# Kernel optimization log

Measured on AMD Instinct MI355X. Metric: run time of the kernel, lower is better.

The kernel has to match this reference:

```python
import jax, jax.numpy as jnp
import numpy as np

B, CH1, CH2, HID, T, E = 64, 3, 4, 16, 16384, 512

def setup_inputs() -> dict:
    key = jax.random.key(0)
    ks = jax.random.split(key, 12)
    s_t = 1.0 / np.sqrt(T)   # fan_in = input_dim for q/k/v projections
    s_e = 1.0 / np.sqrt(E)   # fan_in = embed_dim for out_proj
    return {
        "x":  jax.random.normal(ks[0], (B, 7, T), jnp.float32),
        "W1": jax.random.normal(ks[1], (HID, CH1), jnp.float32) / np.sqrt(CH1),
        "W2": jax.random.normal(ks[2], (HID, CH2), jnp.float32) / np.sqrt(CH2),
        "Wq": jax.random.normal(ks[3], (E, T), jnp.float32) * s_t,
        "bq": jnp.zeros((E,), jnp.float32),
        "Wk": jax.random.normal(ks[4], (E, T), jnp.float32) * s_t,
        "bk": jnp.zeros((E,), jnp.float32),
        "Wv": jax.random.normal(ks[5], (E, T), jnp.float32) * s_t,
        "bv": jnp.zeros((E,), jnp.float32),
        "Wo": jax.random.normal(ks[6], (T, E), jnp.float32) * s_e,
        "bo": jnp.zeros((T,), jnp.float32),
        "W3": jax.random.normal(ks[7], (CH1, HID), jnp.float32) / np.sqrt(HID),
    }

def reference(x, W1, W2, Wq, bq, Wk, bk, Wv, bv, Wo, bo, W3):
    p = x[:, :CH1]            # [B,3,T]  narrow(1,0,ch_1)
    c = x[:, 3:3 + CH2]       # [B,4,T]  narrow(1,3,ch_2)
    q = jnp.einsum('oc,bct->bot', W1, p)   # fc_1: [B,16,T]
    cc = jnp.einsum('oc,bct->bot', W2, c)  # fc_2: [B,16,T]
    # CrossAttention: Linears act on last dim (T -> E)
    Q = jnp.einsum('bct,et->bce', q, Wq) + bq    # [B,16,E]
    K = jnp.einsum('bct,et->bce', cc, Wk) + bk   # [B,16,E]
    V = jnp.einsum('bct,et->bce', cc, Wv) + bv   # [B,16,E]
    scale = 1.0 / np.sqrt(HID)                   # nch = 16 query channels
    attn_w = jax.nn.softmax(jnp.einsum('bce,bcf->bef', Q, K) * scale, axis=-1)  # [B,E,E]
    attn = jnp.einsum('bef,bcf->bce', attn_w, V)  # [B,16,E]
    out = jnp.einsum('bce,te->bct', attn, Wo) + bo  # out_proj: [B,16,T]
    y = jnp.einsum('oc,bct->bot', W3, out)          # fc_3: [B,3,T]
    return p + y
```

## Files before the change

### kernel.cpp

```cpp
#include <hip/hip_runtime.h>

#define BB 64
#define TT 16384
#define EE 512

typedef _Float16 half8 __attribute__((ext_vector_type(8)));
typedef float floatx4 __attribute__((ext_vector_type(4)));

static __device__ __forceinline__ half8 cvt_half8(float4 a, float4 b) {
  half8 h;
  h[0] = (_Float16)a.x; h[1] = (_Float16)a.y; h[2] = (_Float16)a.z; h[3] = (_Float16)a.w;
  h[4] = (_Float16)b.x; h[5] = (_Float16)b.y; h[6] = (_Float16)b.z; h[7] = (_Float16)b.w;
  return h;
}

__global__ __launch_bounds__(256) void zero_ws(float4* __restrict__ p) {
  p[blockIdx.x * 256 + threadIdx.x] = (float4){0.f, 0.f, 0.f, 0.f};
}

__global__ __launch_bounds__(256) void proj_gemm(
    const float* __restrict__ x, const float* __restrict__ Wa,
    const float* __restrict__ Wb, float* __restrict__ outC,
    int chan_base, int chan_per_b, int ldout)
{
  __shared__ _Float16 As[64][40];
  __shared__ _Float16 Bs[128][40];
  const int t = threadIdx.x;
  const int wave = t >> 6, lane = t & 63;
  const int quad = lane >> 4, l16 = lane & 15;
  const int mtile = blockIdx.y, ntile = blockIdx.x;
  const int k0 = blockIdx.z << 10;

  const int arow = t >> 2, akk = (t & 3) << 3;
  const int r = mtile * 64 + arow;
  const int bidx = r / chan_per_b;
  const int j = r - bidx * chan_per_b;
  const float* aptr = x + (size_t)(bidx * 7 + chan_base + j) * TT + k0 + akk;

  const int brow = t >> 1, bkk = (t & 1) << 4;
  const int ncol = ntile * 128 + brow;
  const float* wsrc = (ncol < EE) ? Wa : Wb;
  const float* bptr = wsrc + (size_t)(ncol & (EE - 1)) * TT + k0 + bkk;

  floatx4 acc[4][2];
  for (int rt = 0; rt < 4; ++rt)
    for (int ct = 0; ct < 2; ++ct)
      acc[rt][ct] = (floatx4){0.f, 0.f, 0.f, 0.f};

  for (int kt = 0; kt < 32; ++kt) {
    __syncthreads();
    float4 a0 = *(const float4*)aptr;
    float4 a1 = *(const float4*)(aptr + 4);
    float4 b0 = *(const float4*)bptr;
    float4 b1 = *(const float4*)(bptr + 4);
    float4 b2 = *(const float4*)(bptr + 8);
    float4 b3 = *(const float4*)(bptr + 12);
    *(half8*)&As[arow][akk]     = cvt_half8(a0, a1);
    *(half8*)&Bs[brow][bkk]     = cvt_half8(b0, b1);
    *(half8*)&Bs[brow][bkk + 8] = cvt_half8(b2, b3);
    aptr += 32; bptr += 32;
    __syncthreads();
    half8 bf0 = *(const half8*)&Bs[wave * 32 + l16][quad * 8];
    half8 bf1 = *(const half8*)&Bs[wave * 32 + 16 + l16][quad * 8];
#pragma unroll
    for (int rt = 0; rt < 4; ++rt) {
      half8 af = *(const half8*)&As[rt * 16 + l16][quad * 8];
      acc[rt][0] = __builtin_amdgcn_mfma_f32_16x16x32_f16(af, bf0, acc[rt][0], 0, 0, 0);
      acc[rt][1] = __builtin_amdgcn_mfma_f32_16x16x32_f16(af, bf1, acc[rt][1], 0, 0, 0);
    }
  }
#pragma unroll
  for (int rt = 0; rt < 4; ++rt) {
#pragma unroll
    for (int ct = 0; ct < 2; ++ct) {
      const int gr = mtile * 64 + rt * 16 + quad * 4;
      const int gc = ntile * 128 + wave * 32 + ct * 16 + l16;
#pragma unroll
      for (int rg = 0; rg < 4; ++rg)
        atomicAdd(&outC[(size_t)(gr + rg) * ldout + gc], acc[rt][ct][rg]);
    }
  }
}

__global__ __launch_bounds__(256) void attn_mid(
    const float* __restrict__ Xq, const float* __restrict__ Xkv,
    const float* __restrict__ W1, const float* __restrict__ W2,
    const float* __restrict__ W3,
    const float* __restrict__ bq, const float* __restrict__ bk,
    const float* __restrict__ bv, _Float16* __restrict__ U)
{
  __shared__ float Ks[16][512];
  __shared__ float VW[3][512];
  __shared__ float Qs[16][64];
  __shared__ float Xs[4][512];
  __shared__ float W1s[48], W2s[64], W3s[48], W32s[12], w3sum[3];
  const int t = threadIdx.x;
  const int b = blockIdx.y;
  const int e0 = blockIdx.x * 64;

  if (t < 48) W1s[t] = W1[t];
  if (t >= 64 && t < 128) W2s[t - 64] = W2[t - 64];
  if (t >= 128 && t < 176) W3s[t - 128] = W3[t - 128];
  __syncthreads();
  if (t < 12) {
    const int o = t >> 2, jj = t & 3;
    float s = 0.f;
    for (int c = 0; c < 16; ++c) s += W3s[o * 16 + c] * W2s[c * 4 + jj];
    W32s[t] = s;
  }
  if (t >= 16 && t < 19) {
    const int o = t - 16;
    float s = 0.f;
    for (int c = 0; c < 16; ++c) s += W3s[o * 16 + c];
    w3sum[o] = s;
  }
  for (int i = t; i < 2048; i += 256) {
    const int jj = i >> 9, f = i & 511;
    Xs[jj][f] = Xkv[(size_t)(b * 4 + jj) * 1024 + f];
  }
  __syncthreads();
  for (int i = t; i < 8192; i += 256) {
    const int c = i >> 9, f = i & 511;
    float s = bk[f];
#pragma unroll
    for (int jj = 0; jj < 4; ++jj) s += W2s[c * 4 + jj] * Xs[jj][f];
    Ks[c][f] = s;
  }
  __syncthreads();
  for (int i = t; i < 2048; i += 256) {
    const int jj = i >> 9, f = i & 511;
    Xs[jj][f] = Xkv[(size_t)(b * 4 + jj) * 1024 + 512 + f];
  }
  __syncthreads();
  for (int i = t; i < 1536; i += 256) {
    const int o = i >> 9, f = i & 511;
    float s = w3sum[o] * bv[f];
#pragma unroll
    for (int jj = 0; jj < 4; ++jj) s += W32s[o * 4 + jj] * Xs[jj][f];
    VW[o][f] = s;
  }
  for (int i = t; i < 1024; i += 256) {
    const int c = i >> 6, el = i & 63;
    float s = bq[e0 + el];
#pragma unroll
    for (int jj = 0; jj < 3; ++jj)
      s += W1s[c * 3 + jj] * Xq[(size_t)(b * 3 + jj) * 512 + e0 + el];
    Qs[c][el] = s;
  }
  __syncthreads();

  const int wave = t >> 6, lane = t & 63;
  float vwr[3][8];
#pragma unroll
  for (int o = 0; o < 3; ++o) {
    float4 va = *(const float4*)&VW[o][lane * 8];
    float4 vb = *(const float4*)&VW[o][lane * 8 + 4];
    vwr[o][0] = va.x; vwr[o][1] = va.y; vwr[o][2] = va.z; vwr[o][3] = va.w;
    vwr[o][4] = vb.x; vwr[o][5] = vb.y; vwr[o][6] = vb.z; vwr[o][7] = vb.w;
  }

  for (int g = 0; g < 4; ++g) {
    const int el0 = wave * 16 + g * 4;
    float s[4][8];
#pragma unroll
    for (int e = 0; e < 4; ++e)
#pragma unroll
      for (int i = 0; i < 8; ++i) s[e][i] = 0.f;
#pragma unroll
    for (int c = 0; c < 16; ++c) {
      float4 k0 = *(const float4*)&Ks[c][lane * 8];
      float4 k1 = *(const float4*)&Ks[c][lane * 8 + 4];
      float4 qv = *(const float4*)&Qs[c][el0];
      float qa[4] = {qv.x, qv.y, qv.z, qv.w};
#pragma unroll
      for (int e = 0; e < 4; ++e) {
        const float q = qa[e];
        s[e][0] += q * k0.x; s[e][1] += q * k0.y; s[e][2] += q * k0.z; s[e][3] += q * k0.w;
        s[e][4] += q * k1.x; s[e][5] += q * k1.y; s[e][6] += q * k1.z; s[e][7] += q * k1.w;
      }
    }
#pragma unroll
    for (int e = 0; e < 4; ++e) {
      float mx = s[e][0];
#pragma unroll
      for (int i = 1; i < 8; ++i) mx = fmaxf(mx, s[e][i]);
#pragma unroll
      for (int off = 32; off; off >>= 1) mx = fmaxf(mx, __shfl_xor(mx, off));
      float p[8], sum = 0.f;
#pragma unroll
      for (int i = 0; i < 8; ++i) { p[i] = __expf(0.25f * (s[e][i] - mx)); sum += p[i]; }
      float u0 = 0.f, u1 = 0.f, u2 = 0.f;
#pragma unroll
      for (int i = 0; i < 8; ++i) {
        u0 += p[i] * vwr[0][i];
        u1 += p[i] * vwr[1][i];
        u2 += p[i] * vwr[2][i];
      }
#pragma unroll
      for (int off = 32; off; off >>= 1) {
        sum += __shfl_xor(sum, off);
        u0  += __shfl_xor(u0, off);
        u1  += __shfl_xor(u1, off);
        u2  += __shfl_xor(u2, off);
      }
      if (lane == 0) {
        const float inv = 1.0f / sum;
        const size_t base = (size_t)b * 3 * 512 + (e0 + el0 + e);
        U[base]        = (_Float16)(u0 * inv);
        U[base + 512]  = (_Float16)(u1 * inv);
        U[base + 1024] = (_Float16)(u2 * inv);
      }
    }
  }
}

__global__ __launch_bounds__(256) void out_gemm(
    const _Float16* __restrict__ U, const float* __restrict__ Wo,
    const float* __restrict__ x, const float* __restrict__ bo,
    const float* __restrict__ W3, float* __restrict__ outY)
{
  __shared__ _Float16 As[64][40];
  __shared__ _Float16 Bs[128][40];
  __shared__ float w3sh[3];
  const int t = threadIdx.x;
  const int wave = t >> 6, lane = t & 63;
  const int quad = lane >> 4, l16 = lane & 15;
  const int mtile = blockIdx.y, ntile = blockIdx.x;
  if (t < 3) {
    float s = 0.f;
    for (int c = 0; c < 16; ++c) s += W3[t * 16 + c];
    w3sh[t] = s;
  }
  const int arow = t >> 2, akk = (t & 3) << 3;
  const _Float16* aptr = U + (size_t)(mtile * 64 + arow) * EE + akk;
  const int brow = t >> 1, bkk = (t & 1) << 4;
  const float* bptr = Wo + (size_t)(ntile * 128 + brow) * EE + bkk;

  floatx4 acc[4][2];
  for (int rt = 0; rt < 4; ++rt)
    for (int ct = 0; ct < 2; ++ct)
      acc[rt][ct] = (floatx4){0.f, 0.f, 0.f, 0.f};

  for (int kt = 0; kt < 16; ++kt) {
    __syncthreads();
    half8 av = *(const half8*)aptr;
    float4 b0 = *(const float4*)bptr;
    float4 b1 = *(const float4*)(bptr + 4);
    float4 b2 = *(const float4*)(bptr + 8);
    float4 b3 = *(const float4*)(bptr + 12);
    *(half8*)&As[arow][akk]     = av;
    *(half8*)&Bs[brow][bkk]     = cvt_half8(b0, b1);
    *(half8*)&Bs[brow][bkk + 8] = cvt_half8(b2, b3);
    aptr += 32; bptr += 32;
    __syncthreads();
    half8 bf0 = *(const half8*)&Bs[wave * 32 + l16][quad * 8];
    half8 bf1 = *(const half8*)&Bs[wave * 32 + 16 + l16][quad * 8];
#pragma unroll
    for (int rt = 0; rt < 4; ++rt) {
      half8 af = *(const half8*)&As[rt * 16 + l16][quad * 8];
      acc[rt][0] = __builtin_amdgcn_mfma_f32_16x16x32_f16(af, bf0, acc[rt][0], 0, 0, 0);
      acc[rt][1] = __builtin_amdgcn_mfma_f32_16x16x32_f16(af, bf1, acc[rt][1], 0, 0, 0);
    }
  }
#pragma unroll
  for (int rt = 0; rt < 4; ++rt) {
#pragma unroll
    for (int ct = 0; ct < 2; ++ct) {
      const int gr = mtile * 64 + rt * 16 + quad * 4;
      const int tc = ntile * 128 + wave * 32 + ct * 16 + l16;
      const float bot = bo[tc];
#pragma unroll
      for (int rg = 0; rg < 4; ++rg) {
        const int rr = gr + rg;
        const int bb = rr / 3, oo = rr - bb * 3;
        const float v = acc[rt][ct][rg]
                      + x[(size_t)(bb * 7 + oo) * TT + tc]
                      + w3sh[oo] * bot;
        outY[(size_t)rr * TT + tc] = v;
      }
    }
  }
}

extern "C" void kernel_launch(void* const* d_in, const int* in_sizes, int n_in,
                              void* d_out, int out_size, void* d_ws, size_t ws_size,
                              hipStream_t stream) {
  const float* x  = (const float*)d_in[0];
  const float* W1 = (const float*)d_in[1];
  const float* W2 = (const float*)d_in[2];
  const float* Wq = (const float*)d_in[3];
  const float* bq = (const float*)d_in[4];
  const float* Wk = (const float*)d_in[5];
  const float* bk = (const float*)d_in[6];
  const float* Wv = (const float*)d_in[7];
  const float* bv = (const float*)d_in[8];
  const float* Wo = (const float*)d_in[9];
  const float* bo = (const float*)d_in[10];
  const float* W3 = (const float*)d_in[11];
  float* out = (float*)d_out;

  char* ws = (char*)d_ws;
  float* Xq      = (float*)ws;
  float* Xkv     = (float*)(ws + 393216);
  _Float16* U    = (_Float16*)(ws + 1441792);

  zero_ws<<<dim3(352), 256, 0, stream>>>((float4*)ws);

  proj_gemm<<<dim3(4, 3, 16), 256, 0, stream>>>(x, Wq, Wq, Xq, 0, 3, 512);
  proj_gemm<<<dim3(8, 4, 16), 256, 0, stream>>>(x, Wk, Wv, Xkv, 3, 4, 1024);
  attn_mid<<<dim3(8, BB), 256, 0, stream>>>(Xq, Xkv, W1, W2, W3, bq, bk, bv, U);
  out_gemm<<<dim3(128, 3), 256, 0, stream>>>(U, Wo, x, bo, W3, out);
}
```

Baseline: 314.1 us.

## Merge projection launches, deepen split-K, prefetch tiles, halve out_gemm N-tile

```diff
diff --git a/kernel.cpp b/kernel.cpp
--- a/kernel.cpp
+++ b/kernel.cpp
@@ -19,22 +19,36 @@
 }
 
 __global__ __launch_bounds__(256) void proj_gemm(
-    const float* __restrict__ x, const float* __restrict__ Wa,
-    const float* __restrict__ Wb, float* __restrict__ outC,
-    int chan_base, int chan_per_b, int ldout)
+    const float* __restrict__ x, const float* __restrict__ Wq,
+    const float* __restrict__ Wk, const float* __restrict__ Wv,
+    float* __restrict__ Xq, float* __restrict__ Xkv)
 {
   __shared__ _Float16 As[64][40];
   __shared__ _Float16 Bs[128][40];
   const int t = threadIdx.x;
   const int wave = t >> 6, lane = t & 63;
   const int quad = lane >> 4, l16 = lane & 15;
-  const int mtile = blockIdx.y, ntile = blockIdx.x;
-  const int k0 = blockIdx.z << 10;
+
+  const int tile = blockIdx.x;
+  int mtile, ntile, chan_base, cpb, ldout;
+  const float *Wa, *Wb;
+  float* outC;
+  if (tile < 12) {
+    mtile = tile >> 2; ntile = tile & 3;
+    chan_base = 0; cpb = 3; ldout = 512;
+    Wa = Wq; Wb = Wq; outC = Xq;
+  } else {
+    const int t2 = tile - 12;
+    mtile = t2 >> 3; ntile = t2 & 7;
+    chan_base = 3; cpb = 4; ldout = 1024;
+    Wa = Wk; Wb = Wv; outC = Xkv;
+  }
+  const int k0 = blockIdx.y << 9;
 
   const int arow = t >> 2, akk = (t & 3) << 3;
   const int r = mtile * 64 + arow;
-  const int bidx = r / chan_per_b;
-  const int j = r - bidx * chan_per_b;
+  const int bidx = r / cpb;
+  const int j = r - bidx * cpb;
   const float* aptr = x + (size_t)(bidx * 7 + chan_base + j) * TT + k0 + akk;
 
   const int brow = t >> 1, bkk = (t & 1) << 4;
@@ -47,19 +61,31 @@
     for (int ct = 0; ct < 2; ++ct)
       acc[rt][ct] = (floatx4){0.f, 0.f, 0.f, 0.f};
 
-  for (int kt = 0; kt < 32; ++kt) {
+  float4 a0 = *(const float4*)aptr;
+  float4 a1 = *(const float4*)(aptr + 4);
+  float4 b0 = *(const float4*)bptr;
+  float4 b1 = *(const float4*)(bptr + 4);
+  float4 b2 = *(const float4*)(bptr + 8);
+  float4 b3 = *(const float4*)(bptr + 12);
+
+  for (int kt = 0; kt < 16; ++kt) {
+    const half8 ha  = cvt_half8(a0, a1);
+    const half8 hb0 = cvt_half8(b0, b1);
+    const half8 hb1 = cvt_half8(b2, b3);
     __syncthreads();
-    float4 a0 = *(const float4*)aptr;
-    float4 a1 = *(const float4*)(aptr + 4);
-    float4 b0 = *(const float4*)bptr;
-    float4 b1 = *(const float4*)(bptr + 4);
-    float4 b2 = *(const float4*)(bptr + 8);
-    float4 b3 = *(const float4*)(bptr + 12);
-    *(half8*)&As[arow][akk]     = cvt_half8(a0, a1);
-    *(half8*)&Bs[brow][bkk]     = cvt_half8(b0, b1);
-    *(half8*)&Bs[brow][bkk + 8] = cvt_half8(b2, b3);
-    aptr += 32; bptr += 32;
+    *(half8*)&As[arow][akk]     = ha;
+    *(half8*)&Bs[brow][bkk]     = hb0;
+    *(half8*)&Bs[brow][bkk + 8] = hb1;
     __syncthreads();
+    if (kt < 15) {
+      aptr += 32; bptr += 32;
+      a0 = *(const float4*)aptr;
+      a1 = *(const float4*)(aptr + 4);
+      b0 = *(const float4*)bptr;
+      b1 = *(const float4*)(bptr + 4);
+      b2 = *(const float4*)(bptr + 8);
+      b3 = *(const float4*)(bptr + 12);
+    }
     half8 bf0 = *(const half8*)&Bs[wave * 32 + l16][quad * 8];
     half8 bf1 = *(const half8*)&Bs[wave * 32 + 16 + l16][quad * 8];
 #pragma unroll
@@ -220,7 +246,7 @@
     const float* __restrict__ W3, float* __restrict__ outY)
 {
   __shared__ _Float16 As[64][40];
-  __shared__ _Float16 Bs[128][40];
+  __shared__ _Float16 Bs[64][40];
   __shared__ float w3sh[3];
   const int t = threadIdx.x;
   const int wave = t >> 6, lane = t & 63;
@@ -233,51 +259,49 @@
   }
   const int arow = t >> 2, akk = (t & 3) << 3;
   const _Float16* aptr = U + (size_t)(mtile * 64 + arow) * EE + akk;
-  const int brow = t >> 1, bkk = (t & 1) << 4;
-  const float* bptr = Wo + (size_t)(ntile * 128 + brow) * EE + bkk;
-
-  floatx4 acc[4][2];
-  for (int rt = 0; rt < 4; ++rt)
-    for (int ct = 0; ct < 2; ++ct)
-      acc[rt][ct] = (floatx4){0.f, 0.f, 0.f, 0.f};
+  const int brow = t >> 2, bkk = (t & 3) << 3;
+  const float* bptr = Wo + (size_t)(ntile * 64 + brow) * EE + bkk;
+
+  floatx4 acc[4];
+  for (int rt = 0; rt < 4; ++rt) acc[rt] = (floatx4){0.f, 0.f, 0.f, 0.f};
+
+  half8 av = *(const half8*)aptr;
+  float4 b0 = *(const float4*)bptr;
+  float4 b1 = *(const float4*)(bptr + 4);
 
   for (int kt = 0; kt < 16; ++kt) {
+    const half8 hb = cvt_half8(b0, b1);
+    const half8 ha = av;
     __syncthreads();
-    half8 av = *(const half8*)aptr;
-    float4 b0 = *(const float4*)bptr;
-    float4 b1 = *(const float4*)(bptr + 4);
-    float4 b2 = *(const float4*)(bptr + 8);
-    float4 b3 = *(const float4*)(bptr + 12);
-    *(half8*)&As[arow][akk]     = av;
-    *(half8*)&Bs[brow][bkk]     = cvt_half8(b0, b1);
-    *(half8*)&Bs[brow][bkk + 8] = cvt_half8(b2, b3);
-    aptr += 32; bptr += 32;
+    *(half8*)&As[arow][akk] = ha;
+    *(half8*)&Bs[brow][bkk] = hb;
     __syncthreads();
-    half8 bf0 = *(const half8*)&Bs[wave * 32 + l16][quad * 8];
-    half8 bf1 = *(const half8*)&Bs[wave * 32 + 16 + l16][quad * 8];
+    if (kt < 15) {
+      aptr += 32; bptr += 32;
+      av = *(const half8*)aptr;
+      b0 = *(const float4*)bptr;
+      b1 = *(const float4*)(bptr + 4);
+    }
+    half8 bf = *(const half8*)&Bs[wave * 16 + l16][quad * 8];
 #pragma unroll
     for (int rt = 0; rt < 4; ++rt) {
       half8 af = *(const half8*)&As[rt * 16 + l16][quad * 8];
-      acc[rt][0] = __builtin_amdgcn_mfma_f32_16x16x32_f16(af, bf0, acc[rt][0], 0, 0, 0);
-      acc[rt][1] = __builtin_amdgcn_mfma_f32_16x16x32_f16(af, bf1, acc[rt][1], 0, 0, 0);
+      acc[rt] = __builtin_amdgcn_mfma_f32_16x16x32_f16(af, bf, acc[rt], 0, 0, 0);
     }
   }
 #pragma unroll
   for (int rt = 0; rt < 4; ++rt) {
-#pragma unroll
-    for (int ct = 0; ct < 2; ++ct) {
-      const int gr = mtile * 64 + rt * 16 + quad * 4;
-      const int tc = ntile * 128 + wave * 32 + ct * 16 + l16;
-      const float bot = bo[tc];
-#pragma unroll
-      for (int rg = 0; rg < 4; ++rg) {
-        const int rr = gr + rg;
-        const int bb = rr / 3, oo = rr - bb * 3;
-        const float v = acc[rt][ct][rg]
-                      + x[(size_t)(bb * 7 + oo) * TT + tc]
-                      + w3sh[oo] * bot;
-        outY[(size_t)rr * TT + tc] = v;
-      }
+    const int gr = mtile * 64 + rt * 16 + quad * 4;
+    const int tc = ntile * 64 + wave * 16 + l16;
+    const float bot = bo[tc];
+#pragma unroll
+    for (int rg = 0; rg < 4; ++rg) {
+      const int rr = gr + rg;
+      const int bb = rr / 3, oo = rr - bb * 3;
+      const float v = acc[rt][rg]
+                    + x[(size_t)(bb * 7 + oo) * TT + tc]
+                    + w3sh[oo] * bot;
+      outY[(size_t)rr * TT + tc] = v;
     }
   }
 }
@@ -306,8 +330,7 @@
 
   zero_ws<<<dim3(352), 256, 0, stream>>>((float4*)ws);
 
-  proj_gemm<<<dim3(4, 3, 16), 256, 0, stream>>>(x, Wq, Wq, Xq, 0, 3, 512);
-  proj_gemm<<<dim3(8, 4, 16), 256, 0, stream>>>(x, Wk, Wv, Xkv, 3, 4, 1024);
+  proj_gemm<<<dim3(44, 32), 256, 0, stream>>>(x, Wq, Wk, Wv, Xq, Xkv);
   attn_mid<<<dim3(8, BB), 256, 0, stream>>>(Xq, Xkv, W1, W2, W3, bq, bk, bv, U);
-  out_gemm<<<dim3(128, 3), 256, 0, stream>>>(U, Wo, x, bo, W3, out);
-}
+  out_gemm<<<dim3(256, 3), 256, 0, stream>>>(U, Wo, x, bo, W3, out);
+}
```

Result: faster. 274.1 us (-12.7%).
